# Kernel tuning notes

Measured on AMD Instinct MI355X. Metric: run time of the kernel, lower is better.

The kernel has to match this reference:

```python
import jax, jax.numpy as jnp
import numpy as np

K = 512          # num_embeddings
D = 64           # embedding_dim
BETA = 0.25      # commitment_cost
DECAY = 0.99
EPS = 1e-5


def setup_inputs() -> dict:
    key = jax.random.key(0)
    k1, k2, k3 = jax.random.split(key, 3)
    inputs = jax.random.normal(k1, (64, D, 32, 32), dtype=jnp.float32)  # NCHW, C == embedding_dim
    embedding = jax.random.normal(k2, (K, D), dtype=jnp.float32)
    ema_w = jax.random.normal(k3, (K, D), dtype=jnp.float32)
    ema_cluster_size = jnp.zeros((K,), dtype=jnp.float32)
    return {"inputs": inputs, "embedding": embedding, "ema_w": ema_w,
            "ema_cluster_size": ema_cluster_size}


def reference(inputs, embedding, ema_w, ema_cluster_size):
    # NCHW -> NHWC, flatten to [N, D]
    x = jnp.transpose(inputs, (0, 2, 3, 1))
    B, H, W, C = x.shape
    flat = x.reshape(-1, C)                                   # [N, D]

    # squared L2 distances to all codes: [N, K]
    d = (jnp.sum(flat * flat, axis=1, keepdims=True)
         + jnp.sum(embedding * embedding, axis=1)
         - 2.0 * flat @ embedding.T)
    idx = jnp.argmin(d, axis=1)                               # [N]

    # gather (equivalent to one-hot @ embedding, without materializing one-hot)
    quantized = embedding[idx].reshape(x.shape)               # [B,H,W,D]

    # EMA codebook update (training branch); segment sums replace encodings.T matmuls
    counts = jax.ops.segment_sum(jnp.ones_like(idx, dtype=flat.dtype), idx,
                                 num_segments=K)              # [K]
    new_cs = ema_cluster_size * DECAY + (1.0 - DECAY) * counts
    n = jnp.sum(new_cs)
    new_cs = (new_cs + EPS) / (n + K * EPS) * n               # Laplace smoothing
    dw = jax.ops.segment_sum(flat, idx, num_segments=K)       # [K, D]
    new_ema_w = ema_w * DECAY + (1.0 - DECAY) * dw
    new_embedding = new_ema_w / new_cs[:, None]

    # commitment loss + straight-through estimator
    e_latent_loss = jnp.mean((jax.lax.stop_gradient(quantized) - x) ** 2)
    loss = BETA * e_latent_loss
    quantized_st = x + jax.lax.stop_gradient(quantized - x)

    avg_probs = counts / flat.shape[0]
    perplexity = jnp.exp(-jnp.sum(avg_probs * jnp.log(avg_probs + 1e-10)))

    out_q = jnp.transpose(quantized_st, (0, 3, 1, 2))         # back to NCHW
    return (loss, out_q, perplexity, idx.reshape(B, H, W),
            new_cs, new_ema_w, new_embedding)
```

## Files before the change

### kernel.cpp

```cpp
#include <hip/hip_runtime.h>

#define K_CODES 512
#define DIM 64
#define HW 1024
#define NVEC 65536
#define NREP 4

#define O0 0
#define O1 1
#define O2 4194305
#define O3 4194306
#define O4 4259842
#define O5 4260354
#define O6 4293122

#define WS_LOSS 0
#define WS_EE   512
#define WS_CNT  1024
#define WS_DW   4096
#define WS_BP   135168
#define XSS     72

typedef __bf16 bf16x8 __attribute__((ext_vector_type(8)));
typedef float  f32x4  __attribute__((ext_vector_type(4)));

__global__ void k0_init(const float* __restrict__ emb, float* __restrict__ wsf) {
    const int b = blockIdx.x, t = threadIdx.x;
    if (b < 512) {
        wsf[WS_DW + b * 256 + t] = 0.0f;
    } else if (b == 512) {
        int* cnt = (int*)(wsf + WS_CNT);
        #pragma unroll
        for (int i = 0; i < 8; ++i) cnt[i * 256 + t] = 0;
    } else if (b < 515) {
        int k = (b - 513) * 256 + t;
        const float* e = emb + k * DIM;
        float s = 0.0f;
        #pragma unroll
        for (int c = 0; c < DIM; ++c) s += e[c] * e[c];
        wsf[WS_EE + k] = s;
    } else {
        int g = (b - 515) * 256 + t;
        int j    = g & 7;
        int lane = (g >> 3) & 63;
        int ks   = (g >> 9) & 1;
        int rest = g >> 10;
        int ntg  = rest & 31;
        int s    = rest >> 5;
        int code = ntg * 16 + (lane & 15);
        int c    = ks * 32 + (lane >> 4) * 8 + j;
        float v = -2.0f * emb[code * DIM + c];
        __bf16 h0 = (__bf16)v;  float r1 = v  - (float)h0;
        __bf16 h1 = (__bf16)r1; float r2 = r1 - (float)h1;
        __bf16 hv = (s == 0) ? h0 : (s == 1 ? h1 : (__bf16)r2);
        ((__bf16*)(wsf + WS_BP))[g] = hv;
    }
}

__global__ __launch_bounds__(512, 2)
void k1_main(const float* __restrict__ in, const float* __restrict__ emb,
             float* __restrict__ out, float* __restrict__ wsf) {
    __shared__ float xs[128 * XSS];
    __shared__ float pmin[4][128];
    __shared__ int   pidx[4][128];
    __shared__ float xxs[128];
    __shared__ float lsum[2];
    __shared__ int   hist[K_CODES];

    const int t    = threadIdx.x;
    const int lane = t & 63;
    const int wave = t >> 6;
    const int mi2  = wave & 1;
    const int ni2  = wave >> 1;
    const int col  = lane & 15;
    const int quad = lane >> 4;

    hist[t] = 0;

    const int blk     = blockIdx.x;
    const int rep     = blk & (NREP - 1);
    const int n_img   = blk >> 3;
    const int hw_base = (blk & 7) * 128;
    const float* xbase = in + n_img * (DIM * HW) + hw_base;

    #pragma unroll
    for (int rp = 0; rp < 16; ++rp) {
        int e = rp * 512 + t;
        int c = e >> 7, h0 = e & 127;
        xs[h0 * XSS + c] = xbase[c * HW + h0];
    }

    f32x4 acc[4][8];
    #pragma unroll
    for (int nt = 0; nt < 8; ++nt) {
        float eev = wsf[WS_EE + ni2 * 128 + nt * 16 + col];
        #pragma unroll
        for (int mi = 0; mi < 4; ++mi) {
            acc[mi][nt][0] = eev; acc[mi][nt][1] = eev;
            acc[mi][nt][2] = eev; acc[mi][nt][3] = eev;
        }
    }

    __syncthreads();

    if (t < 128) {
        float s = 0.0f;
        #pragma unroll
        for (int c = 0; c < DIM; ++c) { float v = xs[t * XSS + c]; s += v * v; }
        xxs[t] = s;
    }

    const bf16x8* bp8 = (const bf16x8*)(wsf + WS_BP);

    #pragma unroll
    for (int ks = 0; ks < 2; ++ks) {
        bf16x8 A0[4], A1[4], A2[4];
        #pragma unroll
        for (int mi = 0; mi < 4; ++mi) {
            const float* src = &xs[(mi2 * 64 + mi * 16 + col) * XSS + ks * 32 + quad * 8];
            #pragma unroll
            for (int j = 0; j < 8; ++j) {
                float v = src[j];
                __bf16 h0 = (__bf16)v;  float r1 = v  - (float)h0;
                __bf16 h1 = (__bf16)r1; float r2 = r1 - (float)h1;
                A0[mi][j] = h0; A1[mi][j] = h1; A2[mi][j] = (__bf16)r2;
            }
        }
        #pragma unroll
        for (int s = 0; s < 3; ++s) {
            bf16x8 Bv[8];
            #pragma unroll
            for (int nt = 0; nt < 8; ++nt)
                Bv[nt] = bp8[(((s * 32 + ni2 * 8 + nt) * 2 + ks) * 64) + lane];
            #pragma unroll
            for (int mi = 0; mi < 4; ++mi)
                #pragma unroll
                for (int nt = 0; nt < 8; ++nt)
                    acc[mi][nt] = __builtin_amdgcn_mfma_f32_16x16x32_bf16(A0[mi], Bv[nt], acc[mi][nt], 0, 0, 0);
            if (s < 2) {
                #pragma unroll
                for (int mi = 0; mi < 4; ++mi)
                    #pragma unroll
                    for (int nt = 0; nt < 8; ++nt)
                        acc[mi][nt] = __builtin_amdgcn_mfma_f32_16x16x32_bf16(A1[mi], Bv[nt], acc[mi][nt], 0, 0, 0);
            }
            if (s == 0) {
                #pragma unroll
                for (int mi = 0; mi < 4; ++mi)
                    #pragma unroll
                    for (int nt = 0; nt < 8; ++nt)
                        acc[mi][nt] = __builtin_amdgcn_mfma_f32_16x16x32_bf16(A2[mi], Bv[nt], acc[mi][nt], 0, 0, 0);
            }
        }
    }

    #pragma unroll
    for (int mi = 0; mi < 4; ++mi) {
        #pragma unroll
        for (int r = 0; r < 4; ++r) {
            float v  = acc[mi][0][r];
            int   bi = ni2 * 128 + col;
            #pragma unroll
            for (int nt = 1; nt < 8; ++nt) {
                float u  = acc[mi][nt][r];
                int   ui = ni2 * 128 + nt * 16 + col;
                if (u < v) { v = u; bi = ui; }
            }
            #pragma unroll
            for (int off = 1; off < 16; off <<= 1) {
                float ov = __shfl_xor(v, off);
                int   oi = __shfl_xor(bi, off);
                if (ov < v || (ov == v && oi < bi)) { v = ov; bi = oi; }
            }
            if (col == 0) {
                int row = mi2 * 64 + mi * 16 + quad * 4 + r;
                pmin[ni2][row] = v;
                pidx[ni2][row] = bi;
            }
        }
    }
    __syncthreads();

    if (t < 128) {
        float v = pmin[0][t]; int bi = pidx[0][t];
        #pragma unroll
        for (int q = 1; q < 4; ++q) {
            float u = pmin[q][t]; int ui = pidx[q][t];
            if (u < v) { v = u; bi = ui; }
        }
        pidx[0][t] = bi;
        out[O3 + blk * 128 + t] = (float)bi;
        atomicAdd(&hist[bi], 1);
        float ld = v + xxs[t];
        #pragma unroll
        for (int off = 32; off > 0; off >>= 1) ld += __shfl_down(ld, off);
        if ((t & 63) == 0) lsum[t >> 6] = ld;
    }
    __syncthreads();

    if (t == 0) wsf[WS_LOSS + blk] = lsum[0] + lsum[1];

    {
        int v = t & 127, cq = t >> 7;
        int kv = pidx[0][v];
        const float* ew = emb + kv * DIM;
        float* oq = out + O1 + n_img * (DIM * HW) + hw_base + v;
        #pragma unroll
        for (int c = cq * 16; c < cq * 16 + 16; ++c) oq[c * HW] = ew[c];
    }

    {
        float* dw = wsf + WS_DW + rep * 32768;
        #pragma unroll 1
        for (int v = wave * 16; v < wave * 16 + 16; ++v) {
            int kv = pidx[0][v];
            atomicAdd(&dw[kv * DIM + lane], xs[v * XSS + lane]);
        }
    }

    int* cnt = (int*)(wsf + WS_CNT);
    if (hist[t]) atomicAdd(&cnt[rep * 512 + t], hist[t]);
}

__global__ void k2(const float* __restrict__ ema_cs, const float* __restrict__ ema_w,
                   float* __restrict__ out, const float* __restrict__ wsf) {
    __shared__ float s1[256], s2[256];
    const int t = threadIdx.x;
    const int blk = blockIdx.x;
    const int* cnt = (const int*)(wsf + WS_CNT);

    float ca = 0.0f, cb = 0.0f;
    #pragma unroll
    for (int r = 0; r < NREP; ++r) {
        ca += (float)cnt[r * 512 + t];
        cb += (float)cnt[r * 512 + 256 + t];
    }
    float ra = 0.99f * ema_cs[t]       + 0.01f * ca;
    float rb = 0.99f * ema_cs[256 + t] + 0.01f * cb;
    float pa = ca * (1.0f / 65536.0f);
    float pb = cb * (1.0f / 65536.0f);
    s1[t] = ra + rb;
    s2[t] = pa * logf(pa + 1e-10f) + pb * logf(pb + 1e-10f);
    __syncthreads();
    for (int s = 128; s > 0; s >>= 1) {
        if (t < s) { s1[t] += s1[t + s]; s2[t] += s2[t + s]; }
        __syncthreads();
    }
    const float n = s1[0];
    const float den = n + 512.0f * 1e-5f;

    {
        int m = blk * 256 + t;
        int k = m >> 6;
        float dwsum = wsf[WS_DW + m] + wsf[WS_DW + 32768 + m]
                    + wsf[WS_DW + 65536 + m] + wsf[WS_DW + 98304 + m];
        float w = 0.99f * ema_w[m] + 0.01f * dwsum;
        float ck = 0.0f;
        #pragma unroll
        for (int r = 0; r < NREP; ++r) ck += (float)cnt[r * 512 + k];
        float rawk = 0.99f * ema_cs[k] + 0.01f * ck;
        float csk = (rawk + 1e-5f) / den * n;
        out[O5 + m] = w;
        out[O6 + m] = w / csk;
    }

    if (blk == 0) {
        float s2v = s2[0];
        out[O4 + t]       = (ra + 1e-5f) / den * n;
        out[O4 + 256 + t] = (rb + 1e-5f) / den * n;
        __syncthreads();
        s1[t] = wsf[WS_LOSS + t] + wsf[WS_LOSS + 256 + t];
        __syncthreads();
        for (int s = 128; s > 0; s >>= 1) {
            if (t < s) s1[t] += s1[t + s];
            __syncthreads();
        }
        if (t == 0) {
            out[O0] = 0.25f * s1[0] * (1.0f / 4194304.0f);
            out[O2] = expf(-s2v);
        }
    }
}

extern "C" void kernel_launch(void* const* d_in, const int* in_sizes, int n_in,
                              void* d_out, int out_size, void* d_ws, size_t ws_size,
                              hipStream_t stream) {
    const float* in     = (const float*)d_in[0];
    const float* emb    = (const float*)d_in[1];
    const float* ema_w  = (const float*)d_in[2];
    const float* ema_cs = (const float*)d_in[3];
    float* out = (float*)d_out;
    float* wsf = (float*)d_ws;

    hipLaunchKernelGGL(k0_init, dim3(899), dim3(256), 0, stream, emb, wsf);
    hipLaunchKernelGGL(k1_main, dim3(512), dim3(512), 0, stream, in, emb, out, wsf);
    hipLaunchKernelGGL(k2,      dim3(128), dim3(256), 0, stream, ema_cs, ema_w, out, wsf);
}
```

Measured before the change: 147.7 us.

## Shrink main-kernel tiles to 32 vectors and precompute bf16 splits in shared memory

The main distance/argmin kernel now processes 32 vectors per block with 256 threads across 2048 blocks, replacing 128 vectors per block with 512 threads. Each wave now covers all 32 rows and 128 codes, where before waves were split across rows too. The three-way bf16 split of the inputs is computed once into packed shared-memory arrays and then read as vectors, instead of being recomputed in registers by every wave. The aim is better occupancy and less redundant conversion work. In exchange, each block reloads the full codebook B fragments, giving four times as many codebook reads and loss partials, which k2 now sums over 2048 entries.

```diff
diff --git a/kernel.cpp b/kernel.cpp
--- a/kernel.cpp
+++ b/kernel.cpp
@@ -14,12 +14,11 @@
 #define O5 4260354
 #define O6 4293122
 
-#define WS_LOSS 0
-#define WS_EE   512
-#define WS_CNT  1024
-#define WS_DW   4096
-#define WS_BP   135168
-#define XSS     72
+#define WS_EE   0
+#define WS_CNT  512
+#define WS_LOSS 2560
+#define WS_DW   4608
+#define WS_BP   135680
 
 typedef __bf16 bf16x8 __attribute__((ext_vector_type(8)));
 typedef float  f32x4  __attribute__((ext_vector_type(4)));
@@ -57,45 +56,44 @@
     }
 }
 
-__global__ __launch_bounds__(512, 2)
+__global__ __launch_bounds__(256, 4)
 void k1_main(const float* __restrict__ in, const float* __restrict__ emb,
              float* __restrict__ out, float* __restrict__ wsf) {
-    __shared__ float xs[128 * XSS];
-    __shared__ float pmin[4][128];
-    __shared__ int   pidx[4][128];
-    __shared__ float xxs[128];
-    __shared__ float lsum[2];
+    __shared__ float xs[32 * 65];
+    __shared__ unsigned int xsp[3][32 * 36];
+    __shared__ float pmin[4][32];
+    __shared__ int   pidx[4][32];
+    __shared__ float xxs[32];
     __shared__ int   hist[K_CODES];
 
     const int t    = threadIdx.x;
     const int lane = t & 63;
     const int wave = t >> 6;
-    const int mi2  = wave & 1;
-    const int ni2  = wave >> 1;
+    const int ni   = wave;
     const int col  = lane & 15;
     const int quad = lane >> 4;
 
-    hist[t] = 0;
+    hist[t] = 0; hist[t + 256] = 0;
 
     const int blk     = blockIdx.x;
     const int rep     = blk & (NREP - 1);
-    const int n_img   = blk >> 3;
-    const int hw_base = (blk & 7) * 128;
+    const int n_img   = blk >> 5;
+    const int hw_base = (blk & 31) * 32;
     const float* xbase = in + n_img * (DIM * HW) + hw_base;
 
     #pragma unroll
-    for (int rp = 0; rp < 16; ++rp) {
-        int e = rp * 512 + t;
-        int c = e >> 7, h0 = e & 127;
-        xs[h0 * XSS + c] = xbase[c * HW + h0];
-    }
-
-    f32x4 acc[4][8];
+    for (int it = 0; it < 8; ++it) {
+        int e = it * 256 + t;
+        int c = e >> 5, h = e & 31;
+        xs[h * 65 + c] = xbase[c * HW + h];
+    }
+
+    f32x4 acc[2][8];
     #pragma unroll
     for (int nt = 0; nt < 8; ++nt) {
-        float eev = wsf[WS_EE + ni2 * 128 + nt * 16 + col];
-        #pragma unroll
-        for (int mi = 0; mi < 4; ++mi) {
+        float eev = wsf[WS_EE + ni * 128 + nt * 16 + col];
+        #pragma unroll
+        for (int mi = 0; mi < 2; ++mi) {
             acc[mi][nt][0] = eev; acc[mi][nt][1] = eev;
             acc[mi][nt][2] = eev; acc[mi][nt][3] = eev;
         }
@@ -103,67 +101,89 @@
 
     __syncthreads();
 
-    if (t < 128) {
+    #pragma unroll
+    for (int i = 0; i < 4; ++i) {
+        int e = i * 256 + t;
+        int row = e >> 5, cp = e & 31;
+        float v0 = xs[row * 65 + 2 * cp];
+        float v1 = xs[row * 65 + 2 * cp + 1];
+        __bf16 a0 = (__bf16)v0; float ra = v0 - (float)a0;
+        __bf16 a1 = (__bf16)ra; ra -= (float)a1;
+        __bf16 a2 = (__bf16)ra;
+        __bf16 b0 = (__bf16)v1; float rb = v1 - (float)b0;
+        __bf16 b1 = (__bf16)rb; rb -= (float)b1;
+        __bf16 b2 = (__bf16)rb;
+        union { __bf16 h[2]; unsigned int u; } u0, u1, u2;
+        u0.h[0] = a0; u0.h[1] = b0;
+        u1.h[0] = a1; u1.h[1] = b1;
+        u2.h[0] = a2; u2.h[1] = b2;
+        xsp[0][row * 36 + cp] = u0.u;
+        xsp[1][row * 36 + cp] = u1.u;
+        xsp[2][row * 36 + cp] = u2.u;
+    }
+    if (t < 32) {
         float s = 0.0f;
         #pragma unroll
-        for (int c = 0; c < DIM; ++c) { float v = xs[t * XSS + c]; s += v * v; }
+        for (int c = 0; c < DIM; ++c) { float v = xs[t * 65 + c]; s += v * v; }
         xxs[t] = s;
     }
+    __syncthreads();
 
     const bf16x8* bp8 = (const bf16x8*)(wsf + WS_BP);
 
     #pragma unroll
     for (int ks = 0; ks < 2; ++ks) {
-        bf16x8 A0[4], A1[4], A2[4];
-        #pragma unroll
-        for (int mi = 0; mi < 4; ++mi) {
-            const float* src = &xs[(mi2 * 64 + mi * 16 + col) * XSS + ks * 32 + quad * 8];
+        bf16x8 A0[2], A1[2], A2[2];
+        #pragma unroll
+        for (int mi = 0; mi < 2; ++mi) {
+            int u = (mi * 16 + col) * 36 + ks * 16 + quad * 4;
+            A0[mi] = *(const bf16x8*)&xsp[0][u];
+            A1[mi] = *(const bf16x8*)&xsp[1][u];
+            A2[mi] = *(const bf16x8*)&xsp[2][u];
+        }
+        #pragma unroll
+        for (int s = 0; s < 3; ++s) {
             #pragma unroll
-            for (int j = 0; j < 8; ++j) {
-                float v = src[j];
-                __bf16 h0 = (__bf16)v;  float r1 = v  - (float)h0;
-                __bf16 h1 = (__bf16)r1; float r2 = r1 - (float)h1;
-                A0[mi][j] = h0; A1[mi][j] = h1; A2[mi][j] = (__bf16)r2;
+            for (int bh = 0; bh < 2; ++bh) {
+                bf16x8 Bv[4];
+                #pragma unroll
+                for (int n4 = 0; n4 < 4; ++n4) {
+                    int nt = bh * 4 + n4;
+                    Bv[n4] = bp8[(((s * 32 + ni * 8 + nt) * 2 + ks) * 64) + lane];
+                }
+                #pragma unroll
+                for (int mi = 0; mi < 2; ++mi)
+                    #pragma unroll
+                    for (int n4 = 0; n4 < 4; ++n4)
+                        acc[mi][bh * 4 + n4] = __builtin_amdgcn_mfma_f32_16x16x32_bf16(A0[mi], Bv[n4], acc[mi][bh * 4 + n4], 0, 0, 0);
+                if (s < 2) {
+                    #pragma unroll
+                    for (int mi = 0; mi < 2; ++mi)
+                        #pragma unroll
+                        for (int n4 = 0; n4 < 4; ++n4)
+                            acc[mi][bh * 4 + n4] = __builtin_amdgcn_mfma_f32_16x16x32_bf16(A1[mi], Bv[n4], acc[mi][bh * 4 + n4], 0, 0, 0);
+                }
+                if (s == 0) {
+                    #pragma unroll
+                    for (int mi = 0; mi < 2; ++mi)
+                        #pragma unroll
+                        for (int n4 = 0; n4 < 4; ++n4)
+                            acc[mi][bh * 4 + n4] = __builtin_amdgcn_mfma_f32_16x16x32_bf16(A2[mi], Bv[n4], acc[mi][bh * 4 + n4], 0, 0, 0);
+                }
             }
         }
-        #pragma unroll
-        for (int s = 0; s < 3; ++s) {
-            bf16x8 Bv[8];
-            #pragma unroll
-            for (int nt = 0; nt < 8; ++nt)
-                Bv[nt] = bp8[(((s * 32 + ni2 * 8 + nt) * 2 + ks) * 64) + lane];
-            #pragma unroll
-            for (int mi = 0; mi < 4; ++mi)
-                #pragma unroll
-                for (int nt = 0; nt < 8; ++nt)
-                    acc[mi][nt] = __builtin_amdgcn_mfma_f32_16x16x32_bf16(A0[mi], Bv[nt], acc[mi][nt], 0, 0, 0);
-            if (s < 2) {
-                #pragma unroll
-                for (int mi = 0; mi < 4; ++mi)
-                    #pragma unroll
-                    for (int nt = 0; nt < 8; ++nt)
-                        acc[mi][nt] = __builtin_amdgcn_mfma_f32_16x16x32_bf16(A1[mi], Bv[nt], acc[mi][nt], 0, 0, 0);
-            }
-            if (s == 0) {
-                #pragma unroll
-                for (int mi = 0; mi < 4; ++mi)
-                    #pragma unroll
-                    for (int nt = 0; nt < 8; ++nt)
-                        acc[mi][nt] = __builtin_amdgcn_mfma_f32_16x16x32_bf16(A2[mi], Bv[nt], acc[mi][nt], 0, 0, 0);
-            }
-        }
-    }
-
-    #pragma unroll
-    for (int mi = 0; mi < 4; ++mi) {
+    }
+
+    #pragma unroll
+    for (int mi = 0; mi < 2; ++mi) {
         #pragma unroll
         for (int r = 0; r < 4; ++r) {
             float v  = acc[mi][0][r];
-            int   bi = ni2 * 128 + col;
+            int   bi = ni * 128 + col;
             #pragma unroll
             for (int nt = 1; nt < 8; ++nt) {
                 float u  = acc[mi][nt][r];
-                int   ui = ni2 * 128 + nt * 16 + col;
+                int   ui = ni * 128 + nt * 16 + col;
                 if (u < v) { v = u; bi = ui; }
             }
             #pragma unroll
@@ -173,15 +193,15 @@
                 if (ov < v || (ov == v && oi < bi)) { v = ov; bi = oi; }
             }
             if (col == 0) {
-                int row = mi2 * 64 + mi * 16 + quad * 4 + r;
-                pmin[ni2][row] = v;
-                pidx[ni2][row] = bi;
+                int row = mi * 16 + quad * 4 + r;
+                pmin[ni][row] = v;
+                pidx[ni][row] = bi;
             }
         }
     }
     __syncthreads();
 
-    if (t < 128) {
+    if (t < 32) {
         float v = pmin[0][t]; int bi = pidx[0][t];
         #pragma unroll
         for (int q = 1; q < 4; ++q) {
@@ -189,37 +209,36 @@
             if (u < v) { v = u; bi = ui; }
         }
         pidx[0][t] = bi;
-        out[O3 + blk * 128 + t] = (float)bi;
+        out[O3 + blk * 32 + t] = (float)bi;
         atomicAdd(&hist[bi], 1);
         float ld = v + xxs[t];
         #pragma unroll
-        for (int off = 32; off > 0; off >>= 1) ld += __shfl_down(ld, off);
-        if ((t & 63) == 0) lsum[t >> 6] = ld;
-    }
-    __syncthreads();
-
-    if (t == 0) wsf[WS_LOSS + blk] = lsum[0] + lsum[1];
+        for (int off = 16; off > 0; off >>= 1) ld += __shfl_down(ld, off);
+        if (t == 0) wsf[WS_LOSS + blk] = ld;
+    }
+    __syncthreads();
 
     {
-        int v = t & 127, cq = t >> 7;
+        int v = t & 31, cq = t >> 5;
         int kv = pidx[0][v];
         const float* ew = emb + kv * DIM;
         float* oq = out + O1 + n_img * (DIM * HW) + hw_base + v;
         #pragma unroll
-        for (int c = cq * 16; c < cq * 16 + 16; ++c) oq[c * HW] = ew[c];
+        for (int c = cq * 8; c < cq * 8 + 8; ++c) oq[c * HW] = ew[c];
     }
 
     {
         float* dw = wsf + WS_DW + rep * 32768;
         #pragma unroll 1
-        for (int v = wave * 16; v < wave * 16 + 16; ++v) {
+        for (int v = wave * 8; v < wave * 8 + 8; ++v) {
             int kv = pidx[0][v];
-            atomicAdd(&dw[kv * DIM + lane], xs[v * XSS + lane]);
+            atomicAdd(&dw[kv * DIM + lane], xs[v * 65 + lane]);
         }
     }
 
     int* cnt = (int*)(wsf + WS_CNT);
-    if (hist[t]) atomicAdd(&cnt[rep * 512 + t], hist[t]);
+    if (hist[t])       atomicAdd(&cnt[rep * 512 + t], hist[t]);
+    if (hist[t + 256]) atomicAdd(&cnt[rep * 512 + t + 256], hist[t + 256]);
 }
 
 __global__ void k2(const float* __restrict__ ema_cs, const float* __restrict__ ema_w,
@@ -269,7 +288,10 @@
         out[O4 + t]       = (ra + 1e-5f) / den * n;
         out[O4 + 256 + t] = (rb + 1e-5f) / den * n;
         __syncthreads();
-        s1[t] = wsf[WS_LOSS + t] + wsf[WS_LOSS + 256 + t];
+        float lsum = 0.0f;
+        #pragma unroll
+        for (int j = 0; j < 8; ++j) lsum += wsf[WS_LOSS + j * 256 + t];
+        s1[t] = lsum;
         __syncthreads();
         for (int s = 128; s > 0; s >>= 1) {
             if (t < s) s1[t] += s1[t + s];
@@ -292,7 +314,7 @@
     float* out = (float*)d_out;
     float* wsf = (float*)d_ws;
 
-    hipLaunchKernelGGL(k0_init, dim3(899), dim3(256), 0, stream, emb, wsf);
-    hipLaunchKernelGGL(k1_main, dim3(512), dim3(512), 0, stream, in, emb, out, wsf);
-    hipLaunchKernelGGL(k2,      dim3(128), dim3(256), 0, stream, ema_cs, ema_w, out, wsf);
+    hipLaunchKernelGGL(k0_init, dim3(899),  dim3(256), 0, stream, emb, wsf);
+    hipLaunchKernelGGL(k1_main, dim3(2048), dim3(256), 0, stream, in, emb, out, wsf);
+    hipLaunchKernelGGL(k2,      dim3(128),  dim3(256), 0, stream, ema_cs, ema_w, out, wsf);
 }
```

Result: faster. 137.1 us (-7.2%).
